# Kernel tuning notes

Measured on AMD Instinct MI355X. Metric: run time of the kernel, lower is better.

## Reference

```python
import jax, jax.numpy as jnp
import numpy as np

V, E, H, S = 32000, 1024, 1024, 2048


def setup_inputs() -> dict:
    key = jax.random.key(0)
    k0, k1, k2, k3, k4, k5 = jax.random.split(key, 6)
    tokens = jax.random.randint(k0, (1, S), 0, V)
    emb_table = jax.random.normal(k1, (V, E), jnp.float32) * 0.02
    s = 1.0 / np.sqrt(H)  # PyTorch LSTM default init scale
    W_ih = jax.random.uniform(k2, (4 * H, E), jnp.float32, -s, s)
    W_hh = jax.random.uniform(k3, (4 * H, H), jnp.float32, -s, s)
    b_ih = jax.random.uniform(k4, (4 * H,), jnp.float32, -s, s)
    b_hh = jax.random.uniform(k5, (4 * H,), jnp.float32, -s, s)
    return {"tokens": tokens, "emb_table": emb_table, "W_ih": W_ih,
            "W_hh": W_hh, "b_ih": b_ih, "b_hh": b_hh}


def reference(tokens, emb_table, W_ih, W_hh, b_ih, b_hh):
    # Embed the whole (batch=1) sequence up front: [S, E]
    x = emb_table[tokens[0]]
    hdim = W_hh.shape[1]

    def cell(carry, xt):
        h, c = carry
        # PyTorch gate order: input, forget, cell(g), output
        gates = xt @ W_ih.T + b_ih + h @ W_hh.T + b_hh  # [4H]
        i, f, g, o = jnp.split(gates, 4)
        c = jax.nn.sigmoid(f) * c + jax.nn.sigmoid(i) * jnp.tanh(g)
        h = jax.nn.sigmoid(o) * jnp.tanh(c)
        return (h, c), None

    h0 = jnp.zeros((hdim,), x.dtype)
    c0 = jnp.zeros((hdim,), x.dtype)
    (h, _), _ = jax.lax.scan(cell, (h0, c0), x)
    # encoder_hidden.view(1, -1): final hidden state, shape [1, H]
    return h[None, :]
```

## Files before the change

### kernel.cpp

```cpp
#include <hip/hip_runtime.h>

typedef unsigned int u32_t;

#define S_LEN 2048
#define EDIM  1024
#define HDIM  1024
#define GDIM  4096

#define POISON 0xAAAAAAAAu

__global__ __launch_bounds__(256)
void ix_gemm(const int* __restrict__ tokens, const float* __restrict__ emb,
             const float* __restrict__ Wih, const float* __restrict__ bih,
             const float* __restrict__ bhh, float* __restrict__ ix)
{
    __shared__ float As[16][68];
    __shared__ float Bs[16][68];
    const int t0  = blockIdx.x * 64;
    const int r0  = blockIdx.y * 64;
    const int tid = threadIdx.x;
    const int tx  = tid & 15;
    const int ty  = tid >> 4;
    const int m_a = tid & 63;
    const int k_a = (tid >> 6) << 2;

    const float* arow = emb + (size_t)tokens[t0 + m_a] * EDIM + k_a;
    const float* brow = Wih + (size_t)(r0 + m_a) * EDIM + k_a;

    float acc[4][4] = {};
    for (int kk = 0; kk < EDIM; kk += 16) {
        float4 av = *(const float4*)(arow + kk);
        float4 bv = *(const float4*)(brow + kk);
        __syncthreads();
        As[k_a + 0][m_a] = av.x; As[k_a + 1][m_a] = av.y;
        As[k_a + 2][m_a] = av.z; As[k_a + 3][m_a] = av.w;
        Bs[k_a + 0][m_a] = bv.x; Bs[k_a + 1][m_a] = bv.y;
        Bs[k_a + 2][m_a] = bv.z; Bs[k_a + 3][m_a] = bv.w;
        __syncthreads();
#pragma unroll
        for (int k = 0; k < 16; ++k) {
            float4 a = *(const float4*)&As[k][ty << 2];
            float4 b = *(const float4*)&Bs[k][tx << 2];
            acc[0][0] += a.x * b.x; acc[0][1] += a.x * b.y;
            acc[0][2] += a.x * b.z; acc[0][3] += a.x * b.w;
            acc[1][0] += a.y * b.x; acc[1][1] += a.y * b.y;
            acc[1][2] += a.y * b.z; acc[1][3] += a.y * b.w;
            acc[2][0] += a.z * b.x; acc[2][1] += a.z * b.y;
            acc[2][2] += a.z * b.z; acc[2][3] += a.z * b.w;
            acc[3][0] += a.w * b.x; acc[3][1] += a.w * b.y;
            acc[3][2] += a.w * b.z; acc[3][3] += a.w * b.w;
        }
    }
    const int n0 = r0 + (tx << 2);
    float b0 = bih[n0 + 0] + bhh[n0 + 0];
    float b1 = bih[n0 + 1] + bhh[n0 + 1];
    float b2 = bih[n0 + 2] + bhh[n0 + 2];
    float b3 = bih[n0 + 3] + bhh[n0 + 3];
#pragma unroll
    for (int i = 0; i < 4; ++i) {
        int m = t0 + (ty << 2) + i;
        float4 v = make_float4(acc[i][0] + b0, acc[i][1] + b1,
                               acc[i][2] + b2, acc[i][3] + b3);
        *(float4*)(ix + (size_t)m * GDIM + n0) = v;
    }
}

__device__ __forceinline__ float fast_sigmoid(float x) {
    return 1.0f / (1.0f + __expf(-x));
}
__device__ __forceinline__ float fast_tanh(float x) {
    return 1.0f - 2.0f / (__expf(2.0f * x) + 1.0f);
}

__global__ __launch_bounds__(256)
void lstm_rec(const float* __restrict__ Whh,
              const float* __restrict__ ix,
              u32_t* hslot,
              float* __restrict__ out)
{
    const int tid  = threadIdx.x;
    const int wid  = tid >> 6;
    const int lane = tid & 63;
    const int b    = blockIdx.x;
    const int j    = b * 4 + wid;

    __shared__ float wlds[4][4][HDIM];
    __shared__ float hs[2][HDIM];

#pragma unroll
    for (int w = 0; w < 4; ++w)
#pragma unroll
        for (int g = 0; g < 4; ++g) {
            const float* row = Whh + (size_t)(g * HDIM + b * 4 + w) * HDIM;
            *(float4*)&wlds[w][g][tid << 2] = *(const float4*)(row + (tid << 2));
        }
    __syncthreads();

    float c = 0.0f;
    u32_t p0 = POISON, p1 = POISON, p2 = POISON, p3 = POISON;

    for (int t = 0; t < S_LEN; ++t) {
        const float* ixt = ix + (size_t)t * GDIM;
        float bi = ixt[j];
        float bf = ixt[HDIM + j];
        float bg = ixt[2 * HDIM + j];
        float bo = ixt[3 * HDIM + j];

        const int buf = t & 1;
        if (t == 0) {
            *(float4*)&hs[0][tid << 2] = make_float4(0.f, 0.f, 0.f, 0.f);
        } else {
            const u32_t* src = hslot + (size_t)(t - 1) * HDIM + (tid << 2);
            for (;;) {
                bool m0 = (p0 == POISON), m1 = (p1 == POISON);
                bool m2 = (p2 == POISON), m3 = (p3 == POISON);
                if (!(m0 | m1 | m2 | m3)) break;
                if (m0) p0 = __hip_atomic_load(src + 0, __ATOMIC_RELAXED, __HIP_MEMORY_SCOPE_AGENT);
                if (m1) p1 = __hip_atomic_load(src + 1, __ATOMIC_RELAXED, __HIP_MEMORY_SCOPE_AGENT);
                if (m2) p2 = __hip_atomic_load(src + 2, __ATOMIC_RELAXED, __HIP_MEMORY_SCOPE_AGENT);
                if (m3) p3 = __hip_atomic_load(src + 3, __ATOMIC_RELAXED, __HIP_MEMORY_SCOPE_AGENT);
                __builtin_amdgcn_s_sleep(1);
            }
            *(float4*)&hs[buf][tid << 2] =
                make_float4(__uint_as_float(p0), __uint_as_float(p1),
                            __uint_as_float(p2), __uint_as_float(p3));
        }
        __syncthreads();

        float4 h0 = *(const float4*)&hs[buf][0 * 256 + (lane << 2)];
        float4 h1 = *(const float4*)&hs[buf][1 * 256 + (lane << 2)];
        float4 h2 = *(const float4*)&hs[buf][2 * 256 + (lane << 2)];
        float4 h3 = *(const float4*)&hs[buf][3 * 256 + (lane << 2)];

        float s[4];
#pragma unroll
        for (int g = 0; g < 4; ++g) {
            float4 w0 = *(const float4*)&wlds[wid][g][0 * 256 + (lane << 2)];
            float4 w1 = *(const float4*)&wlds[wid][g][1 * 256 + (lane << 2)];
            float4 w2 = *(const float4*)&wlds[wid][g][2 * 256 + (lane << 2)];
            float4 w3 = *(const float4*)&wlds[wid][g][3 * 256 + (lane << 2)];
            s[g] = w0.x*h0.x + w0.y*h0.y + w0.z*h0.z + w0.w*h0.w
                 + w1.x*h1.x + w1.y*h1.y + w1.z*h1.z + w1.w*h1.w
                 + w2.x*h2.x + w2.y*h2.y + w2.z*h2.z + w2.w*h2.w
                 + w3.x*h3.x + w3.y*h3.y + w3.z*h3.z + w3.w*h3.w;
        }

#pragma unroll
        for (int sh = 32; sh > 0; sh >>= 1) {
            s[0] += __shfl_xor(s[0], sh, 64);
            s[1] += __shfl_xor(s[1], sh, 64);
            s[2] += __shfl_xor(s[2], sh, 64);
            s[3] += __shfl_xor(s[3], sh, 64);
        }

        float si = s[0] + bi, sf = s[1] + bf, sg = s[2] + bg, so = s[3] + bo;
        float ig = fast_sigmoid(si);
        float fg = fast_sigmoid(sf);
        float og = fast_sigmoid(so);
        float gt = fast_tanh(sg);
        c = fg * c + ig * gt;
        float h = og * fast_tanh(c);

        if (lane == 0) {
            u32_t hb = __float_as_uint(h);
            if (hb == POISON) hb = 0u;
            __hip_atomic_store(hslot + (size_t)t * HDIM + j, hb,
                               __ATOMIC_RELAXED, __HIP_MEMORY_SCOPE_AGENT);
            if (t == S_LEN - 1) out[j] = h;
        }

        const u32_t* nsrc = hslot + (size_t)t * HDIM + (tid << 2);
        p0 = __hip_atomic_load(nsrc + 0, __ATOMIC_RELAXED, __HIP_MEMORY_SCOPE_AGENT);
        p1 = __hip_atomic_load(nsrc + 1, __ATOMIC_RELAXED, __HIP_MEMORY_SCOPE_AGENT);
        p2 = __hip_atomic_load(nsrc + 2, __ATOMIC_RELAXED, __HIP_MEMORY_SCOPE_AGENT);
        p3 = __hip_atomic_load(nsrc + 3, __ATOMIC_RELAXED, __HIP_MEMORY_SCOPE_AGENT);
    }
}

extern "C" void kernel_launch(void* const* d_in, const int* in_sizes, int n_in,
                              void* d_out, int out_size, void* d_ws, size_t ws_size,
                              hipStream_t stream) {
    const int*   tokens = (const int*)  d_in[0];
    const float* emb    = (const float*)d_in[1];
    const float* Wih    = (const float*)d_in[2];
    const float* Whh    = (const float*)d_in[3];
    const float* bih    = (const float*)d_in[4];
    const float* bhh    = (const float*)d_in[5];
    float* out = (float*)d_out;

    float* ix    = (float*)d_ws;
    u32_t* hslot = (u32_t*)((char*)d_ws + (size_t)S_LEN * GDIM * 4);

    dim3 gA(S_LEN / 64, GDIM / 64);
    hipLaunchKernelGGL(ix_gemm, gA, dim3(256), 0, stream,
                       tokens, emb, Wih, bih, bhh, ix);
    hipLaunchKernelGGL(lstm_rec, dim3(256), dim3(256), 0, stream,
                       Whh, ix, hslot, out);
}
```

Before: 6.003 ms.

## Pack per-block hidden states into fp16 64-bit atomic slots for cross-block exchange

Each block now gathers its four hidden values in shared memory, converts them to fp16, and publishes them as one 64-bit atomic store. Consumers poll a single 64-bit slot per thread instead of four 32-bit slots, and the s_sleep in the spin loop is dropped. The goal is fewer atomic transactions and lower latency on the per-step cross-block handoff. In exchange it adds an extra __syncthreads per step and rounds h to fp16 across all 2048 recurrent steps, which risks accuracy drift.

```diff
diff --git a/kernel.cpp b/kernel.cpp
--- a/kernel.cpp
+++ b/kernel.cpp
@@ -1,13 +1,15 @@
 #include <hip/hip_runtime.h>
+#include <hip/hip_fp16.h>
 
 typedef unsigned int u32_t;
+typedef unsigned long long u64_t;
 
 #define S_LEN 2048
 #define EDIM  1024
 #define HDIM  1024
 #define GDIM  4096
 
-#define POISON 0xAAAAAAAAu
+#define POISON64 0xAAAAAAAAAAAAAAAAull
 
 __global__ __launch_bounds__(256)
 void ix_gemm(const int* __restrict__ tokens, const float* __restrict__ emb,
@@ -75,7 +77,7 @@
 __global__ __launch_bounds__(256)
 void lstm_rec(const float* __restrict__ Whh,
               const float* __restrict__ ix,
-              u32_t* hslot,
+              u64_t* hq,
               float* __restrict__ out)
 {
     const int tid  = threadIdx.x;
@@ -86,6 +88,7 @@
 
     __shared__ float wlds[4][4][HDIM];
     __shared__ float hs[2][HDIM];
+    __shared__ float hsm[4];
 
 #pragma unroll
     for (int w = 0; w < 4; ++w)
@@ -96,8 +99,8 @@
         }
     __syncthreads();
 
-    float c = 0.0f;
-    u32_t p0 = POISON, p1 = POISON, p2 = POISON, p3 = POISON;
+    float c  = 0.0f;
+    u64_t pv = POISON64;
 
     for (int t = 0; t < S_LEN; ++t) {
         const float* ixt = ix + (size_t)t * GDIM;
@@ -110,20 +113,17 @@
         if (t == 0) {
             *(float4*)&hs[0][tid << 2] = make_float4(0.f, 0.f, 0.f, 0.f);
         } else {
-            const u32_t* src = hslot + (size_t)(t - 1) * HDIM + (tid << 2);
-            for (;;) {
-                bool m0 = (p0 == POISON), m1 = (p1 == POISON);
-                bool m2 = (p2 == POISON), m3 = (p3 == POISON);
-                if (!(m0 | m1 | m2 | m3)) break;
-                if (m0) p0 = __hip_atomic_load(src + 0, __ATOMIC_RELAXED, __HIP_MEMORY_SCOPE_AGENT);
-                if (m1) p1 = __hip_atomic_load(src + 1, __ATOMIC_RELAXED, __HIP_MEMORY_SCOPE_AGENT);
-                if (m2) p2 = __hip_atomic_load(src + 2, __ATOMIC_RELAXED, __HIP_MEMORY_SCOPE_AGENT);
-                if (m3) p3 = __hip_atomic_load(src + 3, __ATOMIC_RELAXED, __HIP_MEMORY_SCOPE_AGENT);
-                __builtin_amdgcn_s_sleep(1);
+            const u64_t* src = hq + (size_t)(t - 1) * 256 + tid;
+            while (pv == POISON64) {
+                pv = __hip_atomic_load(src, __ATOMIC_RELAXED,
+                                       __HIP_MEMORY_SCOPE_AGENT);
             }
+            __half2 lo = *(__half2*)&pv;
+            __half2 hi = *((__half2*)&pv + 1);
+            float2 f01 = __half22float2(lo);
+            float2 f23 = __half22float2(hi);
             *(float4*)&hs[buf][tid << 2] =
-                make_float4(__uint_as_float(p0), __uint_as_float(p1),
-                            __uint_as_float(p2), __uint_as_float(p3));
+                make_float4(f01.x, f01.y, f23.x, f23.y);
         }
         __syncthreads();
 
@@ -162,18 +162,22 @@
         float h = og * fast_tanh(c);
 
         if (lane == 0) {
-            u32_t hb = __float_as_uint(h);
-            if (hb == POISON) hb = 0u;
-            __hip_atomic_store(hslot + (size_t)t * HDIM + j, hb,
+            hsm[wid] = h;
+            if (t == S_LEN - 1) out[j] = h;
+        }
+        __syncthreads();
+
+        if (tid == 0) {
+            __half2 lo = __floats2half2_rn(hsm[0], hsm[1]);
+            __half2 hi = __floats2half2_rn(hsm[2], hsm[3]);
+            u64_t v = (u64_t)*(u32_t*)&lo | ((u64_t)*(u32_t*)&hi << 32);
+            if (v == POISON64) v ^= 1ull;
+            __hip_atomic_store(hq + (size_t)t * 256 + b, v,
                                __ATOMIC_RELAXED, __HIP_MEMORY_SCOPE_AGENT);
-            if (t == S_LEN - 1) out[j] = h;
-        }
-
-        const u32_t* nsrc = hslot + (size_t)t * HDIM + (tid << 2);
-        p0 = __hip_atomic_load(nsrc + 0, __ATOMIC_RELAXED, __HIP_MEMORY_SCOPE_AGENT);
-        p1 = __hip_atomic_load(nsrc + 1, __ATOMIC_RELAXED, __HIP_MEMORY_SCOPE_AGENT);
-        p2 = __hip_atomic_load(nsrc + 2, __ATOMIC_RELAXED, __HIP_MEMORY_SCOPE_AGENT);
-        p3 = __hip_atomic_load(nsrc + 3, __ATOMIC_RELAXED, __HIP_MEMORY_SCOPE_AGENT);
+        }
+
+        pv = __hip_atomic_load(hq + (size_t)t * 256 + tid,
+                               __ATOMIC_RELAXED, __HIP_MEMORY_SCOPE_AGENT);
     }
 }
 
@@ -188,12 +192,12 @@
     const float* bhh    = (const float*)d_in[5];
     float* out = (float*)d_out;
 
-    float* ix    = (float*)d_ws;
-    u32_t* hslot = (u32_t*)((char*)d_ws + (size_t)S_LEN * GDIM * 4);
+    float* ix  = (float*)d_ws;
+    u64_t* hq  = (u64_t*)((char*)d_ws + (size_t)S_LEN * GDIM * 4);
 
     dim3 gA(S_LEN / 64, GDIM / 64);
     hipLaunchKernelGGL(ix_gemm, gA, dim3(256), 0, stream,
                        tokens, emb, Wih, bih, bhh, ix);
     hipLaunchKernelGGL(lstm_rec, dim3(256), dim3(256), 0, stream,
-                       Whh, ix, hslot, out);
-}
+                       Whh, ix, hq, out);
+}
```

Measured after the change: 6.587 ms. +9.7%, slower.

## Poll hidden state per wavefront directly into registers, removing LDS staging barrier

Applied to the files above, without the earlier changes.

Each wavefront now polls all 16 hidden values it needs straight from the global hslot buffer into registers, where before the block split the polling, staged the vector through shared memory and met at a __syncthreads barrier. This removes the block-wide barrier and the LDS round trip on the critical per-timestep path. The cost is four times more atomic global loads per block, since the four wavefronts fetch the same hidden vector redundantly. The per-element spin loops also drop the s_sleep backoff, which may add memory polling pressure.

```diff
diff --git a/kernel.cpp b/kernel.cpp
--- a/kernel.cpp
+++ b/kernel.cpp
@@ -85,7 +85,6 @@
     const int j    = b * 4 + wid;
 
     __shared__ float wlds[4][4][HDIM];
-    __shared__ float hs[2][HDIM];
 
 #pragma unroll
     for (int w = 0; w < 4; ++w)
@@ -97,7 +96,9 @@
     __syncthreads();
 
     float c = 0.0f;
-    u32_t p0 = POISON, p1 = POISON, p2 = POISON, p3 = POISON;
+    u32_t p[16];
+#pragma unroll
+    for (int i = 0; i < 16; ++i) p[i] = POISON;
 
     for (int t = 0; t < S_LEN; ++t) {
         const float* ixt = ix + (size_t)t * GDIM;
@@ -106,31 +107,25 @@
         float bg = ixt[2 * HDIM + j];
         float bo = ixt[3 * HDIM + j];
 
-        const int buf = t & 1;
+        float h[16];
         if (t == 0) {
-            *(float4*)&hs[0][tid << 2] = make_float4(0.f, 0.f, 0.f, 0.f);
+#pragma unroll
+            for (int i = 0; i < 16; ++i) h[i] = 0.0f;
         } else {
-            const u32_t* src = hslot + (size_t)(t - 1) * HDIM + (tid << 2);
-            for (;;) {
-                bool m0 = (p0 == POISON), m1 = (p1 == POISON);
-                bool m2 = (p2 == POISON), m3 = (p3 == POISON);
-                if (!(m0 | m1 | m2 | m3)) break;
-                if (m0) p0 = __hip_atomic_load(src + 0, __ATOMIC_RELAXED, __HIP_MEMORY_SCOPE_AGENT);
-                if (m1) p1 = __hip_atomic_load(src + 1, __ATOMIC_RELAXED, __HIP_MEMORY_SCOPE_AGENT);
-                if (m2) p2 = __hip_atomic_load(src + 2, __ATOMIC_RELAXED, __HIP_MEMORY_SCOPE_AGENT);
-                if (m3) p3 = __hip_atomic_load(src + 3, __ATOMIC_RELAXED, __HIP_MEMORY_SCOPE_AGENT);
-                __builtin_amdgcn_s_sleep(1);
+            const u32_t* src = hslot + (size_t)(t - 1) * HDIM + (lane << 2);
+#pragma unroll
+            for (int m = 0; m < 4; ++m) {
+                const u32_t* s = src + m * 256;
+#pragma unroll
+                for (int i = 0; i < 4; ++i) {
+                    while (p[4 * m + i] == POISON)
+                        p[4 * m + i] = __hip_atomic_load(
+                            s + i, __ATOMIC_RELAXED, __HIP_MEMORY_SCOPE_AGENT);
+                }
             }
-            *(float4*)&hs[buf][tid << 2] =
-                make_float4(__uint_as_float(p0), __uint_as_float(p1),
-                            __uint_as_float(p2), __uint_as_float(p3));
-        }
-        __syncthreads();
-
-        float4 h0 = *(const float4*)&hs[buf][0 * 256 + (lane << 2)];
-        float4 h1 = *(const float4*)&hs[buf][1 * 256 + (lane << 2)];
-        float4 h2 = *(const float4*)&hs[buf][2 * 256 + (lane << 2)];
-        float4 h3 = *(const float4*)&hs[buf][3 * 256 + (lane << 2)];
+#pragma unroll
+            for (int i = 0; i < 16; ++i) h[i] = __uint_as_float(p[i]);
+        }
 
         float s[4];
 #pragma unroll
@@ -139,10 +134,10 @@
             float4 w1 = *(const float4*)&wlds[wid][g][1 * 256 + (lane << 2)];
             float4 w2 = *(const float4*)&wlds[wid][g][2 * 256 + (lane << 2)];
             float4 w3 = *(const float4*)&wlds[wid][g][3 * 256 + (lane << 2)];
-            s[g] = w0.x*h0.x + w0.y*h0.y + w0.z*h0.z + w0.w*h0.w
-                 + w1.x*h1.x + w1.y*h1.y + w1.z*h1.z + w1.w*h1.w
-                 + w2.x*h2.x + w2.y*h2.y + w2.z*h2.z + w2.w*h2.w
-                 + w3.x*h3.x + w3.y*h3.y + w3.z*h3.z + w3.w*h3.w;
+            s[g] = w0.x*h[0]  + w0.y*h[1]  + w0.z*h[2]  + w0.w*h[3]
+                 + w1.x*h[4]  + w1.y*h[5]  + w1.z*h[6]  + w1.w*h[7]
+                 + w2.x*h[8]  + w2.y*h[9]  + w2.z*h[10] + w2.w*h[11]
+                 + w3.x*h[12] + w3.y*h[13] + w3.z*h[14] + w3.w*h[15];
         }
 
 #pragma unroll
@@ -159,21 +154,27 @@
         float og = fast_sigmoid(so);
         float gt = fast_tanh(sg);
         c = fg * c + ig * gt;
-        float h = og * fast_tanh(c);
+        float hv = og * fast_tanh(c);
 
         if (lane == 0) {
-            u32_t hb = __float_as_uint(h);
+            u32_t hb = __float_as_uint(hv);
             if (hb == POISON) hb = 0u;
             __hip_atomic_store(hslot + (size_t)t * HDIM + j, hb,
                                __ATOMIC_RELAXED, __HIP_MEMORY_SCOPE_AGENT);
-            if (t == S_LEN - 1) out[j] = h;
-        }
-
-        const u32_t* nsrc = hslot + (size_t)t * HDIM + (tid << 2);
-        p0 = __hip_atomic_load(nsrc + 0, __ATOMIC_RELAXED, __HIP_MEMORY_SCOPE_AGENT);
-        p1 = __hip_atomic_load(nsrc + 1, __ATOMIC_RELAXED, __HIP_MEMORY_SCOPE_AGENT);
-        p2 = __hip_atomic_load(nsrc + 2, __ATOMIC_RELAXED, __HIP_MEMORY_SCOPE_AGENT);
-        p3 = __hip_atomic_load(nsrc + 3, __ATOMIC_RELAXED, __HIP_MEMORY_SCOPE_AGENT);
+            if (t == S_LEN - 1) out[j] = hv;
+        }
+
+        {
+            const u32_t* nsrc = hslot + (size_t)t * HDIM + (lane << 2);
+#pragma unroll
+            for (int m = 0; m < 4; ++m) {
+#pragma unroll
+                for (int i = 0; i < 4; ++i)
+                    p[4 * m + i] = __hip_atomic_load(
+                        nsrc + m * 256 + i, __ATOMIC_RELAXED,
+                        __HIP_MEMORY_SCOPE_AGENT);
+            }
+        }
     }
 }
 
```

Measured after the change: 21.50 ms. 258% more time.
